# Kernel optimization log

Hardware: AMD Instinct MI355X
Metric: run time of the kernel (lower is better)

The kernel has to match this reference:

```python
import jax, jax.numpy as jnp
import numpy as np

THETA = 2.0  # Clayton generator phi(s) = (1+s)^(-1/theta)
N, F, H = 2_000_000, 64, 32


def _phi(s):
    return jnp.power(1.0 + s, -1.0 / THETA)


def _phi_inv(y):
    # Analytic inverse of the Clayton generator; this is exactly the root
    # newton_root(phi, y) converges to (|phi(t)-y| < tol).
    return jnp.power(y, -THETA) - 1.0


def _log_survival(t, shape, scale, risk):
    return -jnp.exp(risk + shape * jnp.log(t) - shape * jnp.log(scale))


def _log_density(t, shape, scale, risk):
    log_hazard = (risk + shape * jnp.log(t) - shape * jnp.log(scale)
                  + jnp.log(1.0 / t) + jnp.log(shape))
    return log_hazard + _log_survival(t, shape, scale, risk)


def setup_inputs() -> dict:
    key = jax.random.key(0)
    ks = jax.random.split(key, 12)
    x = jax.random.normal(ks[0], (N, F), dtype=jnp.float32)
    t = jax.random.uniform(ks[1], (N,), dtype=jnp.float32) * 10.0 + 0.1  # positive times
    c = (jax.random.uniform(ks[2], (N,), dtype=jnp.float32) < 0.5).astype(jnp.float32)
    s = 0.05
    Wt1 = jax.random.normal(ks[3], (F, H), dtype=jnp.float32) * s
    bt1 = jnp.zeros((H,), dtype=jnp.float32)
    Wt2 = jax.random.normal(ks[4], (H, 1), dtype=jnp.float32) * s
    bt2 = jnp.zeros((1,), dtype=jnp.float32)
    Wc1 = jax.random.normal(ks[5], (F, H), dtype=jnp.float32) * s
    bc1 = jnp.zeros((H,), dtype=jnp.float32)
    Wc2 = jax.random.normal(ks[6], (H, 1), dtype=jnp.float32) * s
    bc2 = jnp.zeros((1,), dtype=jnp.float32)
    shape_t = jnp.ones((), dtype=jnp.float32)
    scale_t = jnp.ones((), dtype=jnp.float32)
    shape_c = jnp.ones((), dtype=jnp.float32)
    scale_c = jnp.ones((), dtype=jnp.float32)
    return dict(x=x, t=t, c=c, Wt1=Wt1, bt1=bt1, Wt2=Wt2, bt2=bt2,
                Wc1=Wc1, bc1=bc1, Wc2=Wc2, bc2=bc2,
                shape_t=shape_t, scale_t=scale_t, shape_c=shape_c, scale_c=scale_c)


def reference(x, t, c, Wt1, bt1, Wt2, bt2, Wc1, bc1, Wc2, bc2,
              shape_t, scale_t, shape_c, scale_c):
    # two-layer linear nets (no nonlinearity, as in the torch module)
    risk_t = ((x @ Wt1 + bt1) @ Wt2 + bt2)[:, 0]  # [N]
    risk_c = ((x @ Wc1 + bc1) @ Wc2 + bc2)[:, 0]  # [N]

    event_log_density = c * _log_density(t, shape_t, scale_t, risk_t)
    censoring_log_density = (1.0 - c) * _log_density(t, shape_c, scale_c, risk_c)

    S_E = jnp.exp(_log_survival(t, shape_t, scale_t, risk_t))
    S_C = jnp.exp(_log_survival(t, shape_c, scale_c, risk_c))
    y = jnp.stack([S_E, S_C], axis=1)  # [N, 2]

    # copula cdf C(y) = phi(phi^{-1}(y1) + phi^{-1}(y2)); cur_k = dC/dy_k.
    # cdf_i depends only on y_i, so grad of the sum gives all per-sample partials.
    def cdf_sum(yy):
        return jnp.sum(_phi(jnp.sum(_phi_inv(yy), axis=1)))

    g = jax.grad(cdf_sum)(y)  # [N, 2]
    cur1, cur2 = g[:, 0], g[:, 1]

    logL = (event_log_density + c * jnp.log(cur1)
            + censoring_log_density + (1.0 - c) * jnp.log(cur2))
    return jnp.sum(logL)
```

## Files before the change

kernel.cpp:

```cpp
#include <hip/hip_runtime.h>

#define HDIM 32
#define FDIM 64

__global__ void prep_kernel(const float* __restrict__ Wt1, const float* __restrict__ bt1,
                            const float* __restrict__ Wt2, const float* __restrict__ bt2,
                            const float* __restrict__ Wc1, const float* __restrict__ bc1,
                            const float* __restrict__ Wc2, const float* __restrict__ bc2,
                            float* __restrict__ ws) {
    int tid = threadIdx.x;
    if (tid < 64) {
        const float* W1 = Wt1 + tid * HDIM;
        float s = 0.f;
        #pragma unroll
        for (int h = 0; h < HDIM; ++h) s = fmaf(W1[h], Wt2[h], s);
        ws[tid] = s;
        if (tid == 0) {
            float b = bt2[0];
            #pragma unroll
            for (int h = 0; h < HDIM; ++h) b = fmaf(bt1[h], Wt2[h], b);
            ws[128] = b;
        }
    } else if (tid < 128) {
        int f = tid - 64;
        const float* W1 = Wc1 + f * HDIM;
        float s = 0.f;
        #pragma unroll
        for (int h = 0; h < HDIM; ++h) s = fmaf(W1[h], Wc2[h], s);
        ws[64 + f] = s;
        if (f == 0) {
            float b = bc2[0];
            #pragma unroll
            for (int h = 0; h < HDIM; ++h) b = fmaf(bc1[h], Wc2[h], b);
            ws[129] = b;
        }
    }
}

__device__ __forceinline__ float row_logl(float rt, float rc, float tv, float cv,
                                          float shape_t, float kt, float lsh_t,
                                          float shape_c, float kc, float lsh_c) {
    float lt  = __logf(tv);
    float u_t = fmaf(shape_t, lt, rt) - kt;
    float u_c = fmaf(shape_c, lt, rc) - kc;
    float e_t = __expf(u_t);
    float e_c = __expf(u_c);
    float ld_t = u_t - lt + lsh_t - e_t;
    float ld_c = u_c - lt + lsh_c - e_c;
    float A    = __expf(2.f * e_t) + __expf(2.f * e_c) - 1.f;
    float logA = __logf(A);
    return cv * (ld_t + 3.f * e_t) + (1.f - cv) * (ld_c + 3.f * e_c) - 1.5f * logA;
}

__launch_bounds__(256, 8)
__global__ void survival_kernel(const float4* __restrict__ x4,
                                const float* __restrict__ t,
                                const float* __restrict__ c,
                                const float* __restrict__ ws,
                                const float* __restrict__ sh_t, const float* __restrict__ sc_t,
                                const float* __restrict__ sh_c, const float* __restrict__ sc_c,
                                float* __restrict__ out, int n) {
    const int tid       = threadIdx.x;
    const int lane      = tid & 63;
    const int sub       = lane & 15;
    const int rowInWave = lane >> 4;
    const int waveId    = tid >> 6;

    const float4 wt = ((const float4*)ws)[sub];
    const float4 wc = ((const float4*)ws)[16 + sub];
    const float bt = ws[128];
    const float bc = ws[129];

    const float shape_t = sh_t[0], scale_t = sc_t[0];
    const float shape_c = sh_c[0], scale_c = sc_c[0];
    const float kt    = shape_t * __logf(scale_t);
    const float kc    = shape_c * __logf(scale_c);
    const float lsh_t = __logf(shape_t);
    const float lsh_c = __logf(shape_c);

    float acc = 0.f;

    const int stride = (int)gridDim.x * 32;
    for (int base = (int)blockIdx.x * 32; base < n; base += stride) {
        int r0 = base + waveId * 8 + rowInWave;
        int r1 = r0 + 4;
        float4 xv0 = make_float4(0.f, 0.f, 0.f, 0.f);
        float4 xv1 = xv0;
        if (r0 < n) xv0 = x4[r0 * 16 + sub];
        if (r1 < n) xv1 = x4[r1 * 16 + sub];

        float pt0 = fmaf(xv0.x, wt.x, fmaf(xv0.y, wt.y, fmaf(xv0.z, wt.z, xv0.w * wt.w)));
        float pc0 = fmaf(xv0.x, wc.x, fmaf(xv0.y, wc.y, fmaf(xv0.z, wc.z, xv0.w * wc.w)));
        float pt1 = fmaf(xv1.x, wt.x, fmaf(xv1.y, wt.y, fmaf(xv1.z, wt.z, xv1.w * wt.w)));
        float pc1 = fmaf(xv1.x, wc.x, fmaf(xv1.y, wc.y, fmaf(xv1.z, wc.z, xv1.w * wc.w)));

        #pragma unroll
        for (int m = 8; m >= 1; m >>= 1) {
            pt0 += __shfl_xor(pt0, m);
            pc0 += __shfl_xor(pc0, m);
            pt1 += __shfl_xor(pt1, m);
            pc1 += __shfl_xor(pc1, m);
        }

        if (sub == 0) {
            if (r0 < n)
                acc += row_logl(pt0 + bt, pc0 + bc, t[r0], c[r0],
                                shape_t, kt, lsh_t, shape_c, kc, lsh_c);
            if (r1 < n)
                acc += row_logl(pt1 + bt, pc1 + bc, t[r1], c[r1],
                                shape_t, kt, lsh_t, shape_c, kc, lsh_c);
        }
    }

    #pragma unroll
    for (int m = 32; m >= 1; m >>= 1) acc += __shfl_xor(acc, m);

    __shared__ float smem[4];
    if (lane == 0) smem[waveId] = acc;
    __syncthreads();
    if (tid == 0) {
        float s = smem[0] + smem[1] + smem[2] + smem[3];
        atomicAdd(out, s);
    }
}

extern "C" void kernel_launch(void* const* d_in, const int* in_sizes, int n_in,
                              void* d_out, int out_size, void* d_ws, size_t ws_size,
                              hipStream_t stream) {
    const float* x   = (const float*)d_in[0];
    const float* t   = (const float*)d_in[1];
    const float* c   = (const float*)d_in[2];
    const float* Wt1 = (const float*)d_in[3];
    const float* bt1 = (const float*)d_in[4];
    const float* Wt2 = (const float*)d_in[5];
    const float* bt2 = (const float*)d_in[6];
    const float* Wc1 = (const float*)d_in[7];
    const float* bc1 = (const float*)d_in[8];
    const float* Wc2 = (const float*)d_in[9];
    const float* bc2 = (const float*)d_in[10];
    const float* sh_t = (const float*)d_in[11];
    const float* sc_t = (const float*)d_in[12];
    const float* sh_c = (const float*)d_in[13];
    const float* sc_c = (const float*)d_in[14];

    float* out = (float*)d_out;
    float* ws  = (float*)d_ws;
    const int n = in_sizes[1];

    hipMemsetAsync(out, 0, sizeof(float), stream);

    prep_kernel<<<1, 128, 0, stream>>>(Wt1, bt1, Wt2, bt2, Wc1, bc1, Wc2, bc2, ws);

    const int grid = 4096;
    survival_kernel<<<grid, 256, 0, stream>>>((const float4*)x, t, c, ws,
                                              sh_t, sc_t, sh_c, sc_c, out, n);
}
```

Baseline: 692.3 us.

## Fuse weight-collapse prep into main kernel and use 4-lane-per-row DPP reduction

Removes the separate prep kernel launch by having every block recompute the collapsed 64-wide weight vectors into shared memory before its row loop. Rows are now handled by 4 lanes each loading four float4s, and the cross-lane sum uses two DPP quad permutes instead of a four-step shuffle tree over 16 lanes. This cuts one kernel launch and most of the shuffle traffic per row. The costs are redundant weight-collapse work in every one of the 4096 blocks, strided per-lane loads that may coalesce less well, and dropping the occupancy hint from the launch bounds.

New measurement: 683.5 us. About the same (-1.3%).

```diff
diff --git a/kernel.cpp b/kernel.cpp
--- a/kernel.cpp
+++ b/kernel.cpp
@@ -3,38 +3,16 @@
 #define HDIM 32
 #define FDIM 64
 
-__global__ void prep_kernel(const float* __restrict__ Wt1, const float* __restrict__ bt1,
-                            const float* __restrict__ Wt2, const float* __restrict__ bt2,
-                            const float* __restrict__ Wc1, const float* __restrict__ bc1,
-                            const float* __restrict__ Wc2, const float* __restrict__ bc2,
-                            float* __restrict__ ws) {
-    int tid = threadIdx.x;
-    if (tid < 64) {
-        const float* W1 = Wt1 + tid * HDIM;
-        float s = 0.f;
-        #pragma unroll
-        for (int h = 0; h < HDIM; ++h) s = fmaf(W1[h], Wt2[h], s);
-        ws[tid] = s;
-        if (tid == 0) {
-            float b = bt2[0];
-            #pragma unroll
-            for (int h = 0; h < HDIM; ++h) b = fmaf(bt1[h], Wt2[h], b);
-            ws[128] = b;
-        }
-    } else if (tid < 128) {
-        int f = tid - 64;
-        const float* W1 = Wc1 + f * HDIM;
-        float s = 0.f;
-        #pragma unroll
-        for (int h = 0; h < HDIM; ++h) s = fmaf(W1[h], Wc2[h], s);
-        ws[64 + f] = s;
-        if (f == 0) {
-            float b = bc2[0];
-            #pragma unroll
-            for (int h = 0; h < HDIM; ++h) b = fmaf(bc1[h], Wc2[h], b);
-            ws[129] = b;
-        }
-    }
+__device__ __forceinline__ float quad_sum(float x) {
+    int v = __builtin_amdgcn_update_dpp(0, __float_as_int(x), 0xB1, 0xF, 0xF, true);
+    x += __int_as_float(v);
+    v = __builtin_amdgcn_update_dpp(0, __float_as_int(x), 0x4E, 0xF, 0xF, true);
+    x += __int_as_float(v);
+    return x;
+}
+
+__device__ __forceinline__ float dot4(float4 a, float4 b) {
+    return fmaf(a.x, b.x, fmaf(a.y, b.y, fmaf(a.z, b.z, a.w * b.w)));
 }
 
 __device__ __forceinline__ float row_logl(float rt, float rc, float tv, float cv,
@@ -52,22 +30,48 @@
     return cv * (ld_t + 3.f * e_t) + (1.f - cv) * (ld_c + 3.f * e_c) - 1.5f * logA;
 }
 
-__launch_bounds__(256, 8)
+__launch_bounds__(256)
 __global__ void survival_kernel(const float4* __restrict__ x4,
                                 const float* __restrict__ t,
-                                const float* __restrict__ c,
-                                const float* __restrict__ ws,
+                                const float* __restrict__ cv,
+                                const float* __restrict__ Wt1, const float* __restrict__ bt1,
+                                const float* __restrict__ Wt2, const float* __restrict__ bt2,
+                                const float* __restrict__ Wc1, const float* __restrict__ bc1,
+                                const float* __restrict__ Wc2, const float* __restrict__ bc2,
                                 const float* __restrict__ sh_t, const float* __restrict__ sc_t,
                                 const float* __restrict__ sh_c, const float* __restrict__ sc_c,
                                 float* __restrict__ out, int n) {
-    const int tid       = threadIdx.x;
-    const int lane      = tid & 63;
-    const int sub       = lane & 15;
-    const int rowInWave = lane >> 4;
-    const int waveId    = tid >> 6;
+    __shared__ __align__(16) float ws[132];
+    __shared__ float wsum[4];
+    const int tid = threadIdx.x;
+    if (tid < 128) {
+        const float* W1 = (tid < 64) ? (Wt1 + tid * HDIM) : (Wc1 + (tid - 64) * HDIM);
+        const float* W2 = (tid < 64) ? Wt2 : Wc2;
+        float s = 0.f;
+        #pragma unroll
+        for (int h = 0; h < HDIM; ++h) s = fmaf(W1[h], W2[h], s);
+        ws[tid] = s;
+    } else if (tid < 130) {
+        const float* b1 = (tid == 128) ? bt1 : bc1;
+        const float* W2 = (tid == 128) ? Wt2 : Wc2;
+        float b = (tid == 128) ? bt2[0] : bc2[0];
+        #pragma unroll
+        for (int h = 0; h < HDIM; ++h) b = fmaf(b1[h], W2[h], b);
+        ws[tid] = b;
+    }
+    __syncthreads();
 
-    const float4 wt = ((const float4*)ws)[sub];
-    const float4 wc = ((const float4*)ws)[16 + sub];
+    const int lane   = tid & 63;
+    const int c4     = lane & 3;
+    const int g      = lane >> 2;
+    const int waveId = tid >> 6;
+    const int rowInBlock = waveId * 16 + g;
+
+    const float4* wsv = (const float4*)ws;
+    const float4 wt0 = wsv[c4],      wt1v = wsv[c4 + 4],
+                 wt2v = wsv[c4 + 8], wt3v = wsv[c4 + 12];
+    const float4 wc0 = wsv[16 + c4],     wc1v = wsv[16 + c4 + 4],
+                 wc2v = wsv[16 + c4 + 8], wc3v = wsv[16 + c4 + 12];
     const float bt = ws[128];
     const float bc = ws[129];
 
@@ -80,48 +84,33 @@
 
     float acc = 0.f;
 
-    const int stride = (int)gridDim.x * 32;
-    for (int base = (int)blockIdx.x * 32; base < n; base += stride) {
-        int r0 = base + waveId * 8 + rowInWave;
-        int r1 = r0 + 4;
-        float4 xv0 = make_float4(0.f, 0.f, 0.f, 0.f);
-        float4 xv1 = xv0;
-        if (r0 < n) xv0 = x4[r0 * 16 + sub];
-        if (r1 < n) xv1 = x4[r1 * 16 + sub];
+    const int stride = (int)gridDim.x * 64;
+    for (int base = (int)blockIdx.x * 64; base < n; base += stride) {
+        const int R = base + rowInBlock;
+        float4 x0 = make_float4(0.f, 0.f, 0.f, 0.f), x1 = x0, x2 = x0, x3 = x0;
+        if (R < n) {
+            const float4* p = x4 + (size_t)R * 16 + c4;
+            x0 = p[0];
+            x1 = p[4];
+            x2 = p[8];
+            x3 = p[12];
+        }
+        float pt = dot4(x0, wt0) + dot4(x1, wt1v) + dot4(x2, wt2v) + dot4(x3, wt3v);
+        float pc = dot4(x0, wc0) + dot4(x1, wc1v) + dot4(x2, wc2v) + dot4(x3, wc3v);
+        pt = quad_sum(pt);
+        pc = quad_sum(pc);
 
-        float pt0 = fmaf(xv0.x, wt.x, fmaf(xv0.y, wt.y, fmaf(xv0.z, wt.z, xv0.w * wt.w)));
-        float pc0 = fmaf(xv0.x, wc.x, fmaf(xv0.y, wc.y, fmaf(xv0.z, wc.z, xv0.w * wc.w)));
-        float pt1 = fmaf(xv1.x, wt.x, fmaf(xv1.y, wt.y, fmaf(xv1.z, wt.z, xv1.w * wt.w)));
-        float pc1 = fmaf(xv1.x, wc.x, fmaf(xv1.y, wc.y, fmaf(xv1.z, wc.z, xv1.w * wc.w)));
-
-        #pragma unroll
-        for (int m = 8; m >= 1; m >>= 1) {
-            pt0 += __shfl_xor(pt0, m);
-            pc0 += __shfl_xor(pc0, m);
-            pt1 += __shfl_xor(pt1, m);
-            pc1 += __shfl_xor(pc1, m);
-        }
-
-        if (sub == 0) {
-            if (r0 < n)
-                acc += row_logl(pt0 + bt, pc0 + bc, t[r0], c[r0],
-                                shape_t, kt, lsh_t, shape_c, kc, lsh_c);
-            if (r1 < n)
-                acc += row_logl(pt1 + bt, pc1 + bc, t[r1], c[r1],
-                                shape_t, kt, lsh_t, shape_c, kc, lsh_c);
+        if (c4 == 0 && R < n) {
+            acc += row_logl(pt + bt, pc + bc, t[R], cv[R],
+                            shape_t, kt, lsh_t, shape_c, kc, lsh_c);
         }
     }
 
     #pragma unroll
     for (int m = 32; m >= 1; m >>= 1) acc += __shfl_xor(acc, m);
-
-    __shared__ float smem[4];
-    if (lane == 0) smem[waveId] = acc;
+    if (lane == 0) wsum[waveId] = acc;
     __syncthreads();
-    if (tid == 0) {
-        float s = smem[0] + smem[1] + smem[2] + smem[3];
-        atomicAdd(out, s);
-    }
+    if (tid == 0) atomicAdd(out, wsum[0] + wsum[1] + wsum[2] + wsum[3]);
 }
 
 extern "C" void kernel_launch(void* const* d_in, const int* in_sizes, int n_in,
@@ -144,14 +133,13 @@
     const float* sc_c = (const float*)d_in[14];
 
     float* out = (float*)d_out;
-    float* ws  = (float*)d_ws;
     const int n = in_sizes[1];
 
     hipMemsetAsync(out, 0, sizeof(float), stream);
 
-    prep_kernel<<<1, 128, 0, stream>>>(Wt1, bt1, Wt2, bt2, Wc1, bc1, Wc2, bc2, ws);
-
     const int grid = 4096;
-    survival_kernel<<<grid, 256, 0, stream>>>((const float4*)x, t, c, ws,
+    survival_kernel<<<grid, 256, 0, stream>>>((const float4*)x, t, c,
+                                              Wt1, bt1, Wt2, bt2,
+                                              Wc1, bc1, Wc2, bc2,
                                               sh_t, sc_t, sh_c, sc_c, out, n);
 }
```
